# Kernel tuning notes

Measured on AMD Instinct MI355X. Metric: run time of the kernel, lower is better.

Reference implementation:

```python
import jax, jax.numpy as jnp
import numpy as np

D_MODEL, D_STATE, EXPAND = 1024, 64, 2
D_INNER = EXPAND * D_MODEL
BATCH, SEQ = 4, 2048


def setup_inputs() -> dict:
    key = jax.random.key(0)
    ks = jax.random.split(key, 7)
    s = lambda *d: 1.0 / np.sqrt(d[0])
    x = jax.random.normal(ks[0], (BATCH, SEQ, D_MODEL), dtype=jnp.float32)
    # weights stored as [in, out] so y = x @ W
    W_in = jax.random.normal(ks[1], (D_MODEL, 2 * D_INNER), dtype=jnp.float32) * s(D_MODEL)
    W_xp = jax.random.normal(ks[2], (D_INNER, 2 * D_STATE + 1), dtype=jnp.float32) * s(D_INNER)
    W_B = jax.random.normal(ks[3], (D_STATE, D_INNER), dtype=jnp.float32) * s(D_STATE)
    W_C = jax.random.normal(ks[4], (D_STATE, D_INNER), dtype=jnp.float32) * s(D_STATE)
    W_out = jax.random.normal(ks[5], (D_INNER, D_MODEL), dtype=jnp.float32) * s(D_INNER)
    D = jnp.ones((D_INNER,), dtype=jnp.float32)
    A_log = jnp.asarray(np.log(0.01), dtype=jnp.float32)
    return {"x": x, "W_in": W_in, "W_xp": W_xp, "W_B": W_B,
            "W_C": W_C, "W_out": W_out, "D": D, "A_log": A_log}


def _scan_recurrence(a, b):
    """h_t = a_t * h_{t-1} + b_t via associative scan over seq axis (axis=1).
    a, b: [B, S, D_inner]."""
    def combine(e1, e2):
        a1, b1 = e1
        a2, b2 = e2
        return a1 * a2, a2 * b1 + b2
    _, h = jax.lax.associative_scan(combine, (a, b), axis=1)
    return h


def reference(x, W_in, W_xp, W_B, W_C, W_out, D, A_log):
    xz = x @ W_in                               # [B,S,2*Di]
    xi, z = jnp.split(xz, 2, axis=-1)           # each [B,S,Di]
    proj = xi @ W_xp                            # [B,S,2*Ds+1]
    delta = jax.nn.softplus(proj[..., :1])      # [B,S,1]
    B_raw = proj[..., 1:1 + D_STATE]
    C_raw = proj[..., 1 + D_STATE:]
    B = B_raw @ W_B                             # [B,S,Di]
    C = C_raw @ W_C                             # [B,S,Di]
    A = -jnp.exp(A_log)                         # scalar
    A_bar = jnp.exp(delta * A)                  # [B,S,1]
    a = jnp.broadcast_to(A_bar, B.shape)        # [B,S,Di]
    h = _scan_recurrence(a, B * xi)             # [B,S,Di]
    y = C * h + D * xi                          # [B,S,Di]
    y = y * jax.nn.silu(z)
    return y @ W_out                            # [B,S,Dm]
```

## Files before the change

kernel.cpp:

```cpp
#include <hip/hip_runtime.h>
#include <hip/hip_bf16.h>
#include <cstdint>
#include <cstddef>

#define D_MODEL 1024
#define D_STATE 64
#define D_INNER 2048
#define BATCH   4
#define SEQ     2048
#define MROWS   (BATCH*SEQ)
#define CHUNK   32
#define NCHUNK  (SEQ/CHUNK)

typedef __bf16 bf16x8 __attribute__((ext_vector_type(8)));
typedef float  f32x4  __attribute__((ext_vector_type(4)));

__device__ __forceinline__ float bf2f(unsigned short u) {
    union { unsigned int i; float f; } v; v.i = ((unsigned int)u) << 16; return v.f;
}
__device__ __forceinline__ unsigned short f2bf(float f) {
    union { float f; unsigned int i; } v; v.f = f;
    unsigned int r = v.i + 0x7fff + ((v.i >> 16) & 1);
    return (unsigned short)(r >> 16);
}
__device__ __forceinline__ float lo16(unsigned u){ return bf2f((unsigned short)(u & 0xffffu)); }
__device__ __forceinline__ float hi16(unsigned u){ return bf2f((unsigned short)(u >> 16)); }
__device__ __forceinline__ unsigned pack2(float a, float b){
    return (unsigned)f2bf(a) | ((unsigned)f2bf(b) << 16);
}

__global__ __launch_bounds__(256) void f32_to_bf16(const float* __restrict__ in,
                                                   unsigned short* __restrict__ out) {
    size_t i = ((size_t)blockIdx.x * 256 + threadIdx.x) * 4;
    float4 v = *(const float4*)(in + i);
    uint2 o; o.x = pack2(v.x, v.y); o.y = pack2(v.z, v.w);
    *(uint2*)(out + i) = o;
}

__global__ void transpose_f32_bf16(const float* __restrict__ in,
                                   unsigned short* __restrict__ out, int rows, int cols) {
    __shared__ float t[32][33];
    int bx = blockIdx.x * 32, by = blockIdx.y * 32;
    int tx = threadIdx.x, ty = threadIdx.y;
    int r = by + ty, c = bx + tx;
    if (r < rows && c < cols) t[ty][tx] = in[(size_t)r * cols + c];
    __syncthreads();
    int ro = bx + ty, co = by + tx;
    if (ro < cols && co < rows) out[(size_t)ro * rows + co] = f2bf(t[tx][ty]);
}

__global__ void transpose_wxp(const float* __restrict__ wxp,
                              unsigned short* __restrict__ out) {
    __shared__ float t[32][33];
    int j0 = blockIdx.x * 32, k0 = blockIdx.y * 32;
    int tx = threadIdx.x, ty = threadIdx.y;
    t[ty][tx] = wxp[(size_t)(k0 + ty) * 129 + 1 + j0 + tx];
    __syncthreads();
    out[(size_t)(j0 + ty) * 2048 + k0 + tx] = f2bf(t[tx][ty]);
}

__global__ void extract_w0(const float* __restrict__ wxp, float* __restrict__ w0f) {
    int k = blockIdx.x * 256 + threadIdx.x;
    if (k < D_INNER) w0f[k] = wxp[(size_t)k * 129];
}

#define BM 128
#define BN 128
#define BK 32
enum { EPI_PLAIN = 0, EPI_MUL_XI = 2, EPI_F32OUT = 3 };

__device__ __forceinline__ void gload_lds16(const void* g, void* l) {
    __builtin_amdgcn_global_load_lds((const __attribute__((address_space(1))) void*)g,
                                     (__attribute__((address_space(3))) void*)l, 16, 0, 0);
}

template<int EPI>
__global__ __launch_bounds__(256) void gemm_tn(
    const unsigned short* __restrict__ A,
    const unsigned short* __restrict__ BT,
    void* __restrict__ Cv,
    const unsigned short* __restrict__ XI, int ldxi,
    int M, int N, int K, int lda, int ldb, int ldc)
{
    __shared__ __align__(16) unsigned short As[BM * BK];
    __shared__ __align__(16) unsigned short Bs[BN * BK];
    const int tid  = threadIdx.x;
    const int wave = tid >> 6, lane = tid & 63;
    const int row0 = blockIdx.y * BM, col0 = blockIdx.x * BN;
    const int wr = (wave >> 1) * 64, wc = (wave & 1) * 64;
    const int srow = lane >> 2;
    const int scol = (lane & 3) * 8;

    f32x4 acc[4][4];
    #pragma unroll
    for (int i = 0; i < 4; ++i)
        #pragma unroll
        for (int j = 0; j < 4; ++j)
            #pragma unroll
            for (int r = 0; r < 4; ++r) acc[i][j][r] = 0.0f;

    for (int k0 = 0; k0 < K; k0 += BK) {
        #pragma unroll
        for (int qi = 0; qi < 2; ++qi) {
            int q = wave * 2 + qi;
            const unsigned short* gA = A  + (size_t)(row0 + q*16 + srow) * lda + (k0 + scol);
            const unsigned short* gB = BT + (size_t)(col0 + q*16 + srow) * ldb + (k0 + scol);
            gload_lds16(gA, &As[q * 512]);
            gload_lds16(gB, &Bs[q * 512]);
        }
        __syncthreads();
        bf16x8 af[4], bfr[4];
        #pragma unroll
        for (int t = 0; t < 4; ++t) {
            af[t]  = *(const bf16x8*)&As[(wr + t*16 + (lane & 15)) * BK + (lane >> 4) * 8];
            bfr[t] = *(const bf16x8*)&Bs[(wc + t*16 + (lane & 15)) * BK + (lane >> 4) * 8];
        }
        #pragma unroll
        for (int i = 0; i < 4; ++i)
            #pragma unroll
            for (int j = 0; j < 4; ++j)
                acc[i][j] = __builtin_amdgcn_mfma_f32_16x16x32_bf16(af[i], bfr[j], acc[i][j], 0, 0, 0);
        __syncthreads();
    }

    const int r0 = (lane >> 4) * 4, cl = lane & 15;
    #pragma unroll
    for (int i = 0; i < 4; ++i) {
        #pragma unroll
        for (int j = 0; j < 4; ++j) {
            #pragma unroll
            for (int r = 0; r < 4; ++r) {
                int gr = row0 + wr + i*16 + r0 + r;
                int gc = col0 + wc + j*16 + cl;
                float v = acc[i][j][r];
                if (EPI == EPI_MUL_XI) v *= bf2f(XI[(size_t)gr * ldxi + gc]);
                if (EPI == EPI_F32OUT) ((float*)Cv)[(size_t)gr * ldc + gc] = v;
                else                   ((unsigned short*)Cv)[(size_t)gr * ldc + gc] = f2bf(v);
            }
        }
    }
}

__global__ __launch_bounds__(256) void delta_kernel(
    const unsigned short* __restrict__ xz, const float* __restrict__ w0f,
    const float* __restrict__ A_log,
    float* __restrict__ dA, float* __restrict__ abar)
{
    int row  = blockIdx.x * 4 + (threadIdx.x >> 6);
    int lane = threadIdx.x & 63;
    const unsigned short* xi = xz + (size_t)row * (2 * D_INNER);
    float s = 0.f;
    #pragma unroll
    for (int step = 0; step < 4; ++step) {
        int oct = step * 64 + lane;
        uint4 u = *(const uint4*)(xi + oct * 8);
        const float4* pw = (const float4*)(w0f + oct * 8);
        float4 wa = pw[0], wb = pw[1];
        s += lo16(u.x)*wa.x + hi16(u.x)*wa.y + lo16(u.y)*wa.z + hi16(u.y)*wa.w
           + lo16(u.z)*wb.x + hi16(u.z)*wb.y + lo16(u.w)*wb.z + hi16(u.w)*wb.w;
    }
    #pragma unroll
    for (int off = 32; off > 0; off >>= 1) s += __shfl_xor(s, off);
    if (lane == 0) {
        float Av = -expf(A_log[0]);
        float d  = (s > 20.f) ? s : log1pf(expf(s));
        float da = d * Av;
        dA[row] = da;
        abar[row] = expf(da);
    }
}

__global__ void chunk_prod(const float* __restrict__ dA, float* __restrict__ P) {
    int idx = threadIdx.x;
    float s = 0.f;
    #pragma unroll
    for (int t = 0; t < CHUNK; ++t) s += dA[idx * CHUNK + t];
    P[idx] = expf(s);
}

__global__ __launch_bounds__(256) void scan_local(
    const unsigned short* __restrict__ bxi, const float* __restrict__ abar,
    float* __restrict__ carry)
{
    int cb = blockIdx.x, j = blockIdx.y, b = blockIdx.z;
    int c0 = cb * 1024 + threadIdx.x * 4;
    int srow = b * SEQ + j * CHUNK;
    const float* ab = abar + srow;
    const unsigned short* p = bxi + (size_t)srow * D_INNER + c0;
    float h0 = 0.f, h1 = 0.f, h2 = 0.f, h3 = 0.f;
    #pragma unroll 8
    for (int t = 0; t < CHUNK; ++t) {
        float a = ab[t];
        uint2 u = *(const uint2*)(p + (size_t)t * D_INNER);
        h0 = fmaf(a, h0, lo16(u.x)); h1 = fmaf(a, h1, hi16(u.x));
        h2 = fmaf(a, h2, lo16(u.y)); h3 = fmaf(a, h3, hi16(u.y));
    }
    *(float4*)(carry + ((size_t)(b * NCHUNK + j)) * D_INNER + c0) = make_float4(h0, h1, h2, h3);
}

__global__ __launch_bounds__(256) void scan_chunks(float* __restrict__ carry,
                                                   const float* __restrict__ P) {
    int c = blockIdx.x * 256 + threadIdx.x;
    int b = blockIdx.y;
    float H = 0.f;
    for (int j = 0; j < NCHUNK; ++j) {
        size_t idx = ((size_t)(b * NCHUNK + j)) * D_INNER + c;
        float cr = carry[idx];
        carry[idx] = H;
        H = P[b * NCHUNK + j] * H + cr;
    }
}

__global__ __launch_bounds__(256) void scan_final(
    const unsigned short* bxi, const unsigned short* __restrict__ cmat,
    const unsigned short* __restrict__ xz, const float* __restrict__ Dvf,
    const float* __restrict__ abar, const float* __restrict__ carry,
    unsigned short* ypre)
{
    int cb = blockIdx.x, j = blockIdx.y, b = blockIdx.z;
    int c0 = cb * 1024 + threadIdx.x * 4;
    int srow = b * SEQ + j * CHUNK;
    float4 hin = *(const float4*)(carry + ((size_t)(b * NCHUNK + j)) * D_INNER + c0);
    float h0 = hin.x, h1 = hin.y, h2 = hin.z, h3 = hin.w;
    float4 dv = *(const float4*)(Dvf + c0);
    float d0 = dv.x, d1 = dv.y, d2 = dv.z, d3 = dv.w;
    const float* ab = abar + srow;
    #pragma unroll 4
    for (int t = 0; t < CHUNK; ++t) {
        size_t m = (size_t)(srow + t);
        float a = ab[t];
        uint2 ub = *(const uint2*)(bxi + m * D_INNER + c0);
        h0 = fmaf(a, h0, lo16(ub.x)); h1 = fmaf(a, h1, hi16(ub.x));
        h2 = fmaf(a, h2, lo16(ub.y)); h3 = fmaf(a, h3, hi16(ub.y));
        uint2 uc = *(const uint2*)(cmat + m * D_INNER + c0);
        uint2 ux = *(const uint2*)(xz + m * (2 * D_INNER) + c0);
        uint2 uz = *(const uint2*)(xz + m * (2 * D_INNER) + D_INNER + c0);
        float y0 = lo16(uc.x) * h0 + d0 * lo16(ux.x);
        float y1 = hi16(uc.x) * h1 + d1 * hi16(ux.x);
        float y2 = lo16(uc.y) * h2 + d2 * lo16(ux.y);
        float y3 = hi16(uc.y) * h3 + d3 * hi16(ux.y);
        float z0 = lo16(uz.x), z1 = hi16(uz.x), z2 = lo16(uz.y), z3 = hi16(uz.y);
        y0 *= z0 / (1.f + expf(-z0)); y1 *= z1 / (1.f + expf(-z1));
        y2 *= z2 / (1.f + expf(-z2)); y3 *= z3 / (1.f + expf(-z3));
        uint2 o; o.x = pack2(y0, y1); o.y = pack2(y2, y3);
        *(uint2*)(ypre + m * D_INNER + c0) = o;
    }
}

extern "C" void kernel_launch(void* const* d_in, const int* in_sizes, int n_in,
                              void* d_out, int out_size, void* d_ws, size_t ws_size,
                              hipStream_t stream) {
    const float* x     = (const float*)d_in[0];
    const float* W_in  = (const float*)d_in[1];
    const float* W_xp  = (const float*)d_in[2];
    const float* W_B   = (const float*)d_in[3];
    const float* W_C   = (const float*)d_in[4];
    const float* W_out = (const float*)d_in[5];
    const float* Dv    = (const float*)d_in[6];
    const float* A_log = (const float*)d_in[7];
    float* out = (float*)d_out;

    size_t off = 0;
    auto alloc = [&](size_t bytes) {
        void* p = (char*)d_ws + off; off += (bytes + 255) & ~(size_t)255; return p;
    };
    unsigned short* xbf   = (unsigned short*)alloc((size_t)MROWS * D_MODEL * 2);
    unsigned short* xz    = (unsigned short*)alloc((size_t)MROWS * 2 * D_INNER * 2);
    unsigned short* bxi   = (unsigned short*)alloc((size_t)MROWS * D_INNER * 2);
    unsigned short* cmat  = (unsigned short*)alloc((size_t)MROWS * D_INNER * 2);
    unsigned short* winT  = (unsigned short*)alloc((size_t)4096 * 1024 * 2);
    unsigned short* woutT = (unsigned short*)alloc((size_t)1024 * 2048 * 2);
    unsigned short* wbT   = (unsigned short*)alloc((size_t)2048 * 64 * 2);
    unsigned short* wcT   = (unsigned short*)alloc((size_t)2048 * 64 * 2);
    unsigned short* wxpT  = (unsigned short*)alloc((size_t)128 * 2048 * 2);
    unsigned short* projb = (unsigned short*)alloc((size_t)MROWS * 128 * 2);
    float* w0f   = (float*)alloc(2048 * 4);
    float* dA    = (float*)alloc(MROWS * 4);
    float* abar  = (float*)alloc(MROWS * 4);
    float* P     = (float*)alloc(BATCH * NCHUNK * 4);
    float* carry = (float*)alloc((size_t)BATCH * NCHUNK * D_INNER * 4);
    (void)ws_size; (void)n_in; (void)in_sizes; (void)out_size;

    hipLaunchKernelGGL(f32_to_bf16, dim3((MROWS * D_MODEL) / 1024), dim3(256), 0, stream, x, xbf);

    dim3 tb(32, 32);
    hipLaunchKernelGGL(transpose_f32_bf16, dim3(4096/32, 1024/32), tb, 0, stream, W_in,  winT, 1024, 4096);
    hipLaunchKernelGGL(transpose_f32_bf16, dim3(1024/32, 2048/32), tb, 0, stream, W_out, woutT, 2048, 1024);
    hipLaunchKernelGGL(transpose_f32_bf16, dim3(2048/32, 64/32),   tb, 0, stream, W_B,   wbT, 64, 2048);
    hipLaunchKernelGGL(transpose_f32_bf16, dim3(2048/32, 64/32),   tb, 0, stream, W_C,   wcT, 64, 2048);
    hipLaunchKernelGGL(transpose_wxp, dim3(4, 64), tb, 0, stream, W_xp, wxpT);
    hipLaunchKernelGGL(extract_w0, dim3(8), dim3(256), 0, stream, W_xp, w0f);

    hipLaunchKernelGGL((gemm_tn<EPI_PLAIN>), dim3(4096/BN, MROWS/BM), dim3(256), 0, stream,
                       xbf, winT, (void*)xz, (const unsigned short*)nullptr, 0,
                       MROWS, 4096, 1024, 1024, 1024, 4096);

    hipLaunchKernelGGL(delta_kernel, dim3(MROWS/4), dim3(256), 0, stream, xz, w0f, A_log, dA, abar);

    hipLaunchKernelGGL((gemm_tn<EPI_PLAIN>), dim3(1, MROWS/BM), dim3(256), 0, stream,
                       xz, wxpT, (void*)projb, (const unsigned short*)nullptr, 0,
                       MROWS, 128, D_INNER, 2*D_INNER, D_INNER, 128);

    hipLaunchKernelGGL((gemm_tn<EPI_MUL_XI>), dim3(D_INNER/BN, MROWS/BM), dim3(256), 0, stream,
                       projb, wbT, (void*)bxi, xz, 2*D_INNER,
                       MROWS, D_INNER, 64, 128, 64, D_INNER);
    hipLaunchKernelGGL((gemm_tn<EPI_PLAIN>), dim3(D_INNER/BN, MROWS/BM), dim3(256), 0, stream,
                       projb + 64, wcT, (void*)cmat, (const unsigned short*)nullptr, 0,
                       MROWS, D_INNER, 64, 128, 64, D_INNER);

    hipLaunchKernelGGL(chunk_prod, dim3(1), dim3(BATCH*NCHUNK), 0, stream, dA, P);
    hipLaunchKernelGGL(scan_local,  dim3(2, NCHUNK, BATCH), dim3(256), 0, stream, bxi, abar, carry);
    hipLaunchKernelGGL(scan_chunks, dim3(D_INNER/256, BATCH), dim3(256), 0, stream, carry, P);
    hipLaunchKernelGGL(scan_final,  dim3(2, NCHUNK, BATCH), dim3(256), 0, stream,
                       bxi, cmat, xz, Dv, abar, carry, bxi );

    hipLaunchKernelGGL((gemm_tn<EPI_F32OUT>), dim3(1024/BN, MROWS/BM), dim3(256), 0, stream,
                       bxi, woutT, (void*)out, (const unsigned short*)nullptr, 0,
                       MROWS, 1024, D_INNER, D_INNER, D_INNER, 1024);
}
```

Baseline: 399.9 us.

## Split-K the x-projection GEMM and deepen GEMM K-step to 64

The narrow x-projection GEMM (N=128, K=2048) launched only 64 blocks. It is now split four ways along K into fp32 partial buffers, and a new reduce kernel sums them into bf16. The shared GEMM template also loads two 32-wide K slices per iteration, which halves the number of barrier/load rounds for every GEMM. The cost is an extra fp32 partial buffer with its write/read traffic, one more launch, and doubled LDS use per block, which could lower occupancy.

```diff
diff --git a/kernel.cpp b/kernel.cpp
--- a/kernel.cpp
+++ b/kernel.cpp
@@ -66,8 +66,7 @@
 
 #define BM 128
 #define BN 128
-#define BK 32
-enum { EPI_PLAIN = 0, EPI_MUL_XI = 2, EPI_F32OUT = 3 };
+enum { EPI_PLAIN = 0, EPI_MUL_XI = 2, EPI_F32OUT = 3, EPI_F32ACC = 4 };
 
 __device__ __forceinline__ void gload_lds16(const void* g, void* l) {
     __builtin_amdgcn_global_load_lds((const __attribute__((address_space(1))) void*)g,
@@ -80,10 +79,12 @@
     const unsigned short* __restrict__ BT,
     void* __restrict__ Cv,
     const unsigned short* __restrict__ XI, int ldxi,
-    int M, int N, int K, int lda, int ldb, int ldc)
+    int M, int N, int kchunk, int lda, int ldb, int ldc)
 {
-    __shared__ __align__(16) unsigned short As[BM * BK];
-    __shared__ __align__(16) unsigned short Bs[BN * BK];
+    __shared__ __align__(16) unsigned short As0[BM * 32];
+    __shared__ __align__(16) unsigned short As1[BM * 32];
+    __shared__ __align__(16) unsigned short Bs0[BN * 32];
+    __shared__ __align__(16) unsigned short Bs1[BN * 32];
     const int tid  = threadIdx.x;
     const int wave = tid >> 6, lane = tid & 63;
     const int row0 = blockIdx.y * BM, col0 = blockIdx.x * BN;
@@ -99,27 +100,35 @@
             #pragma unroll
             for (int r = 0; r < 4; ++r) acc[i][j][r] = 0.0f;
 
-    for (int k0 = 0; k0 < K; k0 += BK) {
+    const int kbeg = blockIdx.z * kchunk;
+    for (int k0 = kbeg; k0 < kbeg + kchunk; k0 += 64) {
         #pragma unroll
         for (int qi = 0; qi < 2; ++qi) {
             int q = wave * 2 + qi;
             const unsigned short* gA = A  + (size_t)(row0 + q*16 + srow) * lda + (k0 + scol);
             const unsigned short* gB = BT + (size_t)(col0 + q*16 + srow) * ldb + (k0 + scol);
-            gload_lds16(gA, &As[q * 512]);
-            gload_lds16(gB, &Bs[q * 512]);
+            gload_lds16(gA,      &As0[q * 512]);
+            gload_lds16(gA + 32, &As1[q * 512]);
+            gload_lds16(gB,      &Bs0[q * 512]);
+            gload_lds16(gB + 32, &Bs1[q * 512]);
         }
         __syncthreads();
-        bf16x8 af[4], bfr[4];
+        bf16x8 af0[4], af1[4], bf0[4], bf1[4];
+        const int lro = lane & 15, lko = (lane >> 4) * 8;
         #pragma unroll
         for (int t = 0; t < 4; ++t) {
-            af[t]  = *(const bf16x8*)&As[(wr + t*16 + (lane & 15)) * BK + (lane >> 4) * 8];
-            bfr[t] = *(const bf16x8*)&Bs[(wc + t*16 + (lane & 15)) * BK + (lane >> 4) * 8];
+            af0[t] = *(const bf16x8*)&As0[(wr + t*16 + lro) * 32 + lko];
+            af1[t] = *(const bf16x8*)&As1[(wr + t*16 + lro) * 32 + lko];
+            bf0[t] = *(const bf16x8*)&Bs0[(wc + t*16 + lro) * 32 + lko];
+            bf1[t] = *(const bf16x8*)&Bs1[(wc + t*16 + lro) * 32 + lko];
         }
         #pragma unroll
         for (int i = 0; i < 4; ++i)
             #pragma unroll
-            for (int j = 0; j < 4; ++j)
-                acc[i][j] = __builtin_amdgcn_mfma_f32_16x16x32_bf16(af[i], bfr[j], acc[i][j], 0, 0, 0);
+            for (int j = 0; j < 4; ++j) {
+                acc[i][j] = __builtin_amdgcn_mfma_f32_16x16x32_bf16(af0[i], bf0[j], acc[i][j], 0, 0, 0);
+                acc[i][j] = __builtin_amdgcn_mfma_f32_16x16x32_bf16(af1[i], bf1[j], acc[i][j], 0, 0, 0);
+            }
         __syncthreads();
     }
 
@@ -134,11 +143,26 @@
                 int gc = col0 + wc + j*16 + cl;
                 float v = acc[i][j][r];
                 if (EPI == EPI_MUL_XI) v *= bf2f(XI[(size_t)gr * ldxi + gc]);
-                if (EPI == EPI_F32OUT) ((float*)Cv)[(size_t)gr * ldc + gc] = v;
-                else                   ((unsigned short*)Cv)[(size_t)gr * ldc + gc] = f2bf(v);
+                if (EPI == EPI_F32OUT)      ((float*)Cv)[(size_t)gr * ldc + gc] = v;
+                else if (EPI == EPI_F32ACC) ((float*)Cv + (size_t)blockIdx.z * M * ldc)[(size_t)gr * ldc + gc] = v;
+                else                        ((unsigned short*)Cv)[(size_t)gr * ldc + gc] = f2bf(v);
             }
         }
     }
+}
+
+__global__ __launch_bounds__(256) void reduce_proj(const float* __restrict__ part,
+                                                   unsigned short* __restrict__ out) {
+    size_t i = ((size_t)blockIdx.x * 256 + threadIdx.x) * 4;
+    const size_t stride = (size_t)MROWS * 128;
+    float4 s = *(const float4*)(part + i);
+    #pragma unroll
+    for (int p = 1; p < 4; ++p) {
+        float4 v = *(const float4*)(part + p * stride + i);
+        s.x += v.x; s.y += v.y; s.z += v.z; s.w += v.w;
+    }
+    uint2 o; o.x = pack2(s.x, s.y); o.y = pack2(s.z, s.w);
+    *(uint2*)(out + i) = o;
 }
 
 __global__ __launch_bounds__(256) void delta_kernel(
@@ -274,6 +298,7 @@
     unsigned short* wcT   = (unsigned short*)alloc((size_t)2048 * 64 * 2);
     unsigned short* wxpT  = (unsigned short*)alloc((size_t)128 * 2048 * 2);
     unsigned short* projb = (unsigned short*)alloc((size_t)MROWS * 128 * 2);
+    float* proj_part = (float*)alloc((size_t)4 * MROWS * 128 * 4);
     float* w0f   = (float*)alloc(2048 * 4);
     float* dA    = (float*)alloc(MROWS * 4);
     float* abar  = (float*)alloc(MROWS * 4);
@@ -297,9 +322,11 @@
 
     hipLaunchKernelGGL(delta_kernel, dim3(MROWS/4), dim3(256), 0, stream, xz, w0f, A_log, dA, abar);
 
-    hipLaunchKernelGGL((gemm_tn<EPI_PLAIN>), dim3(1, MROWS/BM), dim3(256), 0, stream,
-                       xz, wxpT, (void*)projb, (const unsigned short*)nullptr, 0,
-                       MROWS, 128, D_INNER, 2*D_INNER, D_INNER, 128);
+    hipLaunchKernelGGL((gemm_tn<EPI_F32ACC>), dim3(1, MROWS/BM, 4), dim3(256), 0, stream,
+                       xz, wxpT, (void*)proj_part, (const unsigned short*)nullptr, 0,
+                       MROWS, 128, 512, 2*D_INNER, D_INNER, 128);
+    hipLaunchKernelGGL(reduce_proj, dim3((MROWS * 128) / 1024), dim3(256), 0, stream,
+                       proj_part, projb);
 
     hipLaunchKernelGGL((gemm_tn<EPI_MUL_XI>), dim3(D_INNER/BN, MROWS/BM), dim3(256), 0, stream,
                        projb, wbT, (void*)bxi, xz, 2*D_INNER,
@@ -316,5 +343,5 @@
 
     hipLaunchKernelGGL((gemm_tn<EPI_F32OUT>), dim3(1024/BN, MROWS/BM), dim3(256), 0, stream,
                        bxi, woutT, (void*)out, (const unsigned short*)nullptr, 0,
-                       MROWS, 1024, D_INNER, D_INNER, D_INNER, 1024);
-}
+                       MROWS, 1024, 2048, D_INNER, D_INNER, 1024);
+}
```

After: 363.1 us. 1.1x faster.
